# Performance work log

Hardware: AMD Instinct MI355X
Metric: run time of the kernel (lower is better)

Reference implementation:

```python
import jax, jax.numpy as jnp
import numpy as np

TOP_K = 2
LN_EPS = 1e-6


def setup_inputs() -> dict:
    key = jax.random.key(0)
    ks = jax.random.split(key, 8)
    B, T, D, FF, E = 4, 512, 1024, 4096, 8
    x = jax.random.normal(ks[0], (B, T, D), dtype=jnp.float32)
    gate_w = jax.random.normal(ks[1], (E, D), dtype=jnp.float32) * (1.0 / np.sqrt(D))
    ln_g = jnp.ones((E, D), dtype=jnp.float32)
    ln_b = jnp.zeros((E, D), dtype=jnp.float32)
    w1 = jax.random.normal(ks[2], (E, FF, D), dtype=jnp.float32) * (1.0 / np.sqrt(D))
    b1 = jnp.zeros((E, FF), dtype=jnp.float32)
    w2 = jax.random.normal(ks[3], (E, D, FF), dtype=jnp.float32) * (1.0 / np.sqrt(FF))
    b2 = jnp.zeros((E, D), dtype=jnp.float32)
    return {"x": x, "gate_w": gate_w, "ln_g": ln_g, "ln_b": ln_b,
            "w1": w1, "b1": b1, "w2": w2, "b2": b2}


def reference(x, gate_w, ln_g, ln_b, w1, b1, w2, b2):
    B, T, D = x.shape
    E = gate_w.shape[0]
    N = B * T
    xf = x.reshape(N, D)

    # ---- Router: linear gate -> softmax -> top-k dispatch mask + aux loss ----
    logits = xf @ gate_w.T                          # [N, E]
    scores = jax.nn.softmax(logits, axis=-1)        # [N, E]
    topk_vals, topk_idx = jax.lax.top_k(scores, TOP_K)
    dispatch = jnp.zeros_like(scores).at[
        jnp.arange(N)[:, None], topk_idx].set(1.0)  # [N, E] 0/1 mask
    load = dispatch.sum(axis=0)                     # [E]
    importance = scores.sum(axis=0)                 # [E]
    aux_loss = (importance * load).sum() * E / (N * N)

    # ---- Experts (PositionwiseFeedForward, kernel_size=1, skip connection) ----
    # Dense-all-experts compute, masked combine: identical math to the
    # per-expert gather/scatter loop in the torch module.
    mu = xf.mean(axis=-1, keepdims=True)
    var = ((xf - mu) ** 2).mean(axis=-1, keepdims=True)
    norm = (xf - mu) / jnp.sqrt(var + LN_EPS)       # [N, D]
    xe = norm[:, None, :] * ln_g[None] + ln_b[None] # [N, E, D] per-expert LN
    h = jax.nn.relu(jnp.einsum('ned,efd->nef', xe, w1) + b1[None])  # [N, E, FF]
    y = jnp.einsum('nef,edf->ned', h, w2) + b2[None] + xf[:, None, :]  # +skip

    comb = scores * dispatch                        # top-k gate weights [N, E]
    out = jnp.einsum('ne,ned->nd', comb, y).reshape(B, T, D)
    return out, aux_loss
```

## Files before the change

### kernel.cpp

```cpp
#include <hip/hip_runtime.h>
#include <hip/hip_bf16.h>

#define N_TOK 2048
#define DMODEL 1024
#define NEXP 8
#define FFDIM 4096
#define NMAX 2048
#define PADROWS 5120
#define TMAX 40

#define BM 128
#define BN 128
#define BK 64
#define KSPL 4

typedef __attribute__((ext_vector_type(8))) short s16x8;
typedef __attribute__((ext_vector_type(4))) float f32x4;

__device__ __forceinline__ float bf2f(ushort u) {
    union { uint i; float f; } x; x.i = ((uint)u) << 16; return x.f;
}
__device__ __forceinline__ ushort f2bf(float f) {
    union { float f; uint i; } x; x.f = f;
    uint r = x.i + 0x7fffu + ((x.i >> 16) & 1u);
    return (ushort)(r >> 16);
}

__device__ __forceinline__ void gl_lds16(const void* g, void* l) {
    __builtin_amdgcn_global_load_lds(
        (const __attribute__((address_space(1))) unsigned int*)g,
        (__attribute__((address_space(3))) unsigned int*)l, 16, 0, 0);
}

__device__ __forceinline__ float block_sum(float v, float* s4) {
    #pragma unroll
    for (int off = 32; off; off >>= 1) v += __shfl_down(v, off);
    __syncthreads();
    if ((threadIdx.x & 63) == 0) s4[threadIdx.x >> 6] = v;
    __syncthreads();
    return s4[0] + s4[1] + s4[2] + s4[3];
}

__global__ __launch_bounds__(256)
void router_kernel(const float* __restrict__ x, const float* __restrict__ gate_w,
                   ushort* __restrict__ norm, float* __restrict__ scores,
                   int* __restrict__ cnt, int* __restrict__ lists,
                   int4* __restrict__ info, float2* __restrict__ gpair) {
    __shared__ float s4[4];
    const int n = blockIdx.x, tid = threadIdx.x;
    const float* xr = x + (size_t)n * DMODEL;
    float4 v = *(const float4*)(xr + tid * 4);

    float tot = block_sum(v.x + v.y + v.z + v.w, s4);
    float mu = tot * (1.0f / DMODEL);
    float d0 = v.x - mu, d1 = v.y - mu, d2 = v.z - mu, d3 = v.w - mu;
    float var = block_sum(d0 * d0 + d1 * d1 + d2 * d2 + d3 * d3, s4) * (1.0f / DMODEL);
    float rstd = rsqrtf(var + 1e-6f);

    ushort nb[4] = { f2bf(d0 * rstd), f2bf(d1 * rstd), f2bf(d2 * rstd), f2bf(d3 * rstd) };
    *(uint2*)(norm + (size_t)n * DMODEL + tid * 4) = *(uint2*)nb;

    float lg[NEXP];
    #pragma unroll
    for (int e = 0; e < NEXP; ++e) {
        float4 g = *(const float4*)(gate_w + (size_t)e * DMODEL + tid * 4);
        lg[e] = v.x * g.x + v.y * g.y + v.z * g.z + v.w * g.w;
    }
    #pragma unroll
    for (int e = 0; e < NEXP; ++e) lg[e] = block_sum(lg[e], s4);

    if (tid == 0) {
        float m = lg[0];
        #pragma unroll
        for (int e = 1; e < NEXP; ++e) m = fmaxf(m, lg[e]);
        float ex[NEXP], Z = 0.f;
        #pragma unroll
        for (int e = 0; e < NEXP; ++e) { ex[e] = expf(lg[e] - m); Z += ex[e]; }
        float inv = 1.0f / Z;
        float sc[NEXP];
        #pragma unroll
        for (int e = 0; e < NEXP; ++e) { sc[e] = ex[e] * inv; scores[n * NEXP + e] = sc[e]; }
        int i1 = 0;
        #pragma unroll
        for (int e = 1; e < NEXP; ++e) if (sc[e] > sc[i1]) i1 = e;
        int i2 = (i1 == 0) ? 1 : 0;
        #pragma unroll
        for (int e = 0; e < NEXP; ++e) if (e != i1 && sc[e] > sc[i2]) i2 = e;
        int s1 = atomicAdd(&cnt[i1], 1);
        lists[i1 * NMAX + s1] = n;
        int s2 = atomicAdd(&cnt[i2], 1);
        lists[i2 * NMAX + s2] = n;
        info[n] = make_int4(i1, s1, i2, s2);
        gpair[n] = make_float2(sc[i1], sc[i2]);
    }
}

__global__ __launch_bounds__(256)
void prep_kernel(const float* __restrict__ scores, const int* __restrict__ cnt,
                 int* __restrict__ offs_pad, int* __restrict__ ntiles,
                 int4* __restrict__ tilemap, float* __restrict__ aux_out) {
    __shared__ float s4[4];
    __shared__ float imp[NEXP];
    float part[NEXP] = {};
    for (int i = threadIdx.x; i < N_TOK; i += 256) {
        #pragma unroll
        for (int e = 0; e < NEXP; ++e) part[e] += scores[i * NEXP + e];
    }
    #pragma unroll
    for (int e = 0; e < NEXP; ++e) {
        float s = block_sum(part[e], s4);
        if (threadIdx.x == 0) imp[e] = s;
    }
    __syncthreads();
    if (threadIdx.x == 0) {
        float aux = 0.f; int pad = 0, idx = 0;
        #pragma unroll
        for (int e = 0; e < NEXP; ++e) {
            aux += imp[e] * (float)cnt[e];
            offs_pad[e] = pad;
            int tiles = (cnt[e] + BM - 1) / BM;
            for (int t = 0; t < tiles; ++t)
                tilemap[idx++] = make_int4(e, pad + t * BM, 0, 0);
            pad += tiles * BM;
        }
        offs_pad[NEXP] = pad;
        ntiles[0] = idx;
        aux_out[0] = aux * (float)NEXP / ((float)N_TOK * (float)N_TOK);
    }
}

__global__ __launch_bounds__(256)
void gather_kernel(const ushort* __restrict__ norm, const float* __restrict__ ln_g,
                   const float* __restrict__ ln_b, const int* __restrict__ offs_pad,
                   const int* __restrict__ cnt, const int* __restrict__ lists,
                   ushort* __restrict__ A1) {
    const int r = blockIdx.x;
    int e = 0;
    #pragma unroll
    for (int k = 1; k < NEXP; ++k) if (r >= offs_pad[k]) e = k;
    const int slot = r - offs_pad[e];
    const int t4 = threadIdx.x * 4;
    if (slot >= cnt[e]) {
        ushort z[4] = {};
        *(uint2*)(A1 + (size_t)r * DMODEL + t4) = *(uint2*)z;
        return;
    }
    const int token = lists[e * NMAX + slot];
    uint2 nbv = *(const uint2*)(norm + (size_t)token * DMODEL + t4);
    ushort ns[4]; *(uint2*)ns = nbv;
    float4 gv = *(const float4*)(ln_g + (size_t)e * DMODEL + t4);
    float4 bv = *(const float4*)(ln_b + (size_t)e * DMODEL + t4);
    ushort ob[4] = { f2bf(bf2f(ns[0]) * gv.x + bv.x), f2bf(bf2f(ns[1]) * gv.y + bv.y),
                     f2bf(bf2f(ns[2]) * gv.z + bv.z), f2bf(bf2f(ns[3]) * gv.w + bv.w) };
    *(uint2*)(A1 + (size_t)r * DMODEL + t4) = *(uint2*)ob;
}

template<int KDIM, int NT, int KSPLT, bool RELU>
__global__ __launch_bounds__(256, 2)
void moe_gemm(const ushort* __restrict__ A, const float* __restrict__ W,
              const float* __restrict__ bias, const int* __restrict__ ntiles,
              const int4* __restrict__ tilemap, ushort* __restrict__ hout,
              float* __restrict__ yout) {
    __shared__ ushort As[2][BM * BK];
    __shared__ ushort Ws[2][BN * BK];
    constexpr int NOUT = NT * BN;

    const int q = (int)gridDim.x >> 3;
    const int logical = ((int)blockIdx.x & 7) * q + ((int)blockIdx.x >> 3);
    const int bt = logical % TMAX;
    int g = logical / TMAX;
    if (bt >= ntiles[0]) return;
    const int nt = g % NT;
    const int kb = g / NT;
    const int4 tm = tilemap[bt];
    const int e = tm.x, row0 = tm.y;

    const int tid = threadIdx.x, lane = tid & 63, wave = tid >> 6;
    const int wm = (wave & 1) * 64, wn = (wave >> 1) * 64;
    const int trow = lane >> 3;
    const int scol = ((lane & 7) ^ trow) * 8;

    const ushort* Agb = A + (size_t)row0 * KDIM;
    const float*  Wgb = W + ((size_t)e * NOUT + nt * BN) * KDIM;

    f32x4 acc[4][4] = {};
    float4 wr[8];

    auto loadWreg = [&](int step) {
        #pragma unroll
        for (int i = 0; i < 4; ++i) {
            int c = tid + 256 * i;
            const float* p = Wgb + (size_t)(c >> 3) * KDIM + step * BK + (c & 7) * 8;
            wr[2 * i]     = *(const float4*)p;
            wr[2 * i + 1] = *(const float4*)(p + 4);
        }
    };
    auto stageA = [&](int step, int b) {
        #pragma unroll
        for (int i = 0; i < 4; ++i) {
            int c = wave * 4 + i;
            gl_lds16(Agb + (size_t)(c * 8 + trow) * KDIM + step * BK + scol, &As[b][c * 512]);
        }
    };
    auto cvtWriteW = [&](int b) {
        #pragma unroll
        for (int i = 0; i < 4; ++i) {
            int c = tid + 256 * i;
            int row = c >> 3, col8 = (c & 7) * 8;
            union { s16x8 v; __hip_bfloat162 h2[4]; } u;
            u.h2[0] = __float22bfloat162_rn(make_float2(wr[2 * i].x, wr[2 * i].y));
            u.h2[1] = __float22bfloat162_rn(make_float2(wr[2 * i].z, wr[2 * i].w));
            u.h2[2] = __float22bfloat162_rn(make_float2(wr[2 * i + 1].x, wr[2 * i + 1].y));
            u.h2[3] = __float22bfloat162_rn(make_float2(wr[2 * i + 1].z, wr[2 * i + 1].w));
            *(s16x8*)&Ws[b][row * BK + (col8 ^ ((row & 7) << 3))] = u.v;
        }
    };
    auto mfma_phase = [&](int b) {
        #pragma unroll
        for (int kki = 0; kki < 2; ++kki) {
            const int cx = (kki * 32 + (lane >> 4) * 8) ^ ((lane & 7) << 3);
            s16x8 af[4], bfv[4];
            #pragma unroll
            for (int mi = 0; mi < 4; ++mi)
                af[mi] = *(const s16x8*)&As[b][(wm + mi * 16 + (lane & 15)) * BK + cx];
            #pragma unroll
            for (int ni = 0; ni < 4; ++ni)
                bfv[ni] = *(const s16x8*)&Ws[b][(wn + ni * 16 + (lane & 15)) * BK + cx];
            #pragma unroll
            for (int mi = 0; mi < 4; ++mi)
                #pragma unroll
                for (int ni = 0; ni < 4; ++ni)
                    acc[mi][ni] = __builtin_amdgcn_mfma_f32_16x16x32_bf16(
                        af[mi], bfv[ni], acc[mi][ni], 0, 0, 0);
        }
    };

    const int KS = KDIM / BK / KSPLT;
    const int kt0 = kb * KS;

    loadWreg(kt0);
    stageA(kt0, 0);
    cvtWriteW(0);
    asm volatile("s_waitcnt vmcnt(0) lgkmcnt(0)" ::: "memory");
    __builtin_amdgcn_s_barrier();
    __builtin_amdgcn_sched_barrier(0);

    int buf = 0;
    for (int s = 0; s < KS; ++s) {
        if (s + 1 < KS) {
            loadWreg(kt0 + s + 1);
            __builtin_amdgcn_sched_barrier(0);
            stageA(kt0 + s + 1, buf ^ 1);
            __builtin_amdgcn_sched_barrier(0);
        }
        mfma_phase(buf);
        __builtin_amdgcn_sched_barrier(0);
        if (s + 1 < KS) cvtWriteW(buf ^ 1);
        asm volatile("s_waitcnt vmcnt(0) lgkmcnt(0)" ::: "memory");
        __builtin_amdgcn_sched_barrier(0);
        __builtin_amdgcn_s_barrier();
        __builtin_amdgcn_sched_barrier(0);
        buf ^= 1;
    }

    if (RELU) {
        #pragma unroll
        for (int ni = 0; ni < 4; ++ni) {
            const int nn = nt * BN + wn + ni * 16 + (lane & 15);
            const float bv = bias[(size_t)e * NOUT + nn];
            #pragma unroll
            for (int mi = 0; mi < 4; ++mi)
                #pragma unroll
                for (int r = 0; r < 4; ++r) {
                    const int sl = wm + mi * 16 + ((lane >> 4) << 2) + r;
                    hout[(size_t)(row0 + sl) * NOUT + nn] =
                        f2bf(fmaxf(acc[mi][ni][r] + bv, 0.f));
                }
        }
    } else {
        #pragma unroll
        for (int ni = 0; ni < 4; ++ni) {
            const int nn = nt * BN + wn + ni * 16 + (lane & 15);
            #pragma unroll
            for (int mi = 0; mi < 4; ++mi)
                #pragma unroll
                for (int r = 0; r < 4; ++r) {
                    const int sl = wm + mi * 16 + ((lane >> 4) << 2) + r;
                    yout[((size_t)kb * PADROWS + row0 + sl) * NOUT + nn] = acc[mi][ni][r];
                }
        }
    }
}

__global__ __launch_bounds__(256)
void combine_kernel(const float* __restrict__ ypart, const float* __restrict__ b2,
                    const float* __restrict__ x, const int* __restrict__ offs_pad,
                    const int4* __restrict__ info, const float2* __restrict__ gpair,
                    float* __restrict__ out) {
    const int n = blockIdx.x, d = threadIdx.x * 4;
    const int4 ii = info[n];
    const float2 g = gpair[n];
    const int r1 = offs_pad[ii.x] + ii.y, r2 = offs_pad[ii.z] + ii.w;
    f32x4 y1 = {}, y2 = {};
    #pragma unroll
    for (int kb = 0; kb < KSPL; ++kb) {
        y1 += *(const f32x4*)(ypart + ((size_t)kb * PADROWS + r1) * DMODEL + d);
        y2 += *(const f32x4*)(ypart + ((size_t)kb * PADROWS + r2) * DMODEL + d);
    }
    const f32x4 b21 = *(const f32x4*)(b2 + (size_t)ii.x * DMODEL + d);
    const f32x4 b22 = *(const f32x4*)(b2 + (size_t)ii.z * DMODEL + d);
    const f32x4 xv  = *(const f32x4*)(x + (size_t)n * DMODEL + d);
    f32x4 o = g.x * (y1 + b21 + xv) + g.y * (y2 + b22 + xv);
    *(f32x4*)(out + (size_t)n * DMODEL + d) = o;
}

extern "C" void kernel_launch(void* const* d_in, const int* in_sizes, int n_in,
                              void* d_out, int out_size, void* d_ws, size_t ws_size,
                              hipStream_t stream) {
    const float* x      = (const float*)d_in[0];
    const float* gate_w = (const float*)d_in[1];
    const float* ln_g   = (const float*)d_in[2];
    const float* ln_b   = (const float*)d_in[3];
    const float* w1     = (const float*)d_in[4];
    const float* b1     = (const float*)d_in[5];
    const float* w2     = (const float*)d_in[6];
    const float* b2     = (const float*)d_in[7];
    float* out = (float*)d_out;

    char* w = (char*)d_ws;
    int*    cnt      = (int*)(w + 0);
    int*    offs_pad = (int*)(w + 64);
    int*    ntiles   = (int*)(w + 128);
    int4*   tilemap  = (int4*)(w + 192);
    int*    lists    = (int*)(w + 1024);
    float*  scores   = (float*)(w + 66560);
    int4*   info     = (int4*)(w + 132096);
    float2* gpair    = (float2*)(w + 164864);
    ushort* norm     = (ushort*)(w + 181248);
    ushort* A1       = (ushort*)(w + 4375552);
    ushort* h        = (ushort*)(w + 14861312);
    float*  ypart    = (float*)(w + 56804352);

    hipMemsetAsync(cnt, 0, 64, stream);

    router_kernel<<<N_TOK, 256, 0, stream>>>(x, gate_w, norm, scores, cnt, lists, info, gpair);
    prep_kernel<<<1, 256, 0, stream>>>(scores, cnt, offs_pad, ntiles, tilemap,
                                       out + (size_t)N_TOK * DMODEL);
    gather_kernel<<<PADROWS, 256, 0, stream>>>(norm, ln_g, ln_b, offs_pad, cnt, lists, A1);
    moe_gemm<DMODEL, FFDIM / BN, 1, true><<<TMAX * (FFDIM / BN), 256, 0, stream>>>(
        A1, w1, b1, ntiles, tilemap, h, nullptr);
    moe_gemm<FFDIM, DMODEL / BN, KSPL, false><<<TMAX * (DMODEL / BN) * KSPL, 256, 0, stream>>>(
        h, w2, nullptr, ntiles, tilemap, nullptr, ypart);
    combine_kernel<<<N_TOK, 256, 0, stream>>>(ypart, b2, x, offs_pad, info, gpair, out);
}
```

Measured before the change: 299.6 us.

## Stream fp32 weights straight to LDS and convert at fragment read; one token per wave in router

The GEMM no longer loads fp32 weights into registers and converts them before writing to LDS. It stages them directly into swizzled fp32 LDS with global_load_lds and converts to bf16 when building MFMA fragments. BK is halved to 32 so the fp32 tile fits, occupancy is raised to 3 blocks per CU, and the prefetch now waits with a partial vmcnt so it overlaps the MFMA phase. The router handles one token per wave with shuffle reductions in place of block-level barriers. The trade-off is more k-steps, more barriers per unit of work, and a conversion inside the MFMA loop.

```diff
diff --git a/kernel.cpp b/kernel.cpp
--- a/kernel.cpp
+++ b/kernel.cpp
@@ -11,7 +11,7 @@
 
 #define BM 128
 #define BN 128
-#define BK 64
+#define BK 32
 #define KSPL 4
 
 typedef __attribute__((ext_vector_type(8))) short s16x8;
@@ -30,6 +30,12 @@
     __builtin_amdgcn_global_load_lds(
         (const __attribute__((address_space(1))) unsigned int*)g,
         (__attribute__((address_space(3))) unsigned int*)l, 16, 0, 0);
+}
+
+__device__ __forceinline__ float wave_sum(float v) {
+    #pragma unroll
+    for (int off = 32; off; off >>= 1) v += __shfl_xor(v, off);
+    return v;
 }
 
 __device__ __forceinline__ float block_sum(float v, float* s4) {
@@ -46,30 +52,52 @@
                    ushort* __restrict__ norm, float* __restrict__ scores,
                    int* __restrict__ cnt, int* __restrict__ lists,
                    int4* __restrict__ info, float2* __restrict__ gpair) {
-    __shared__ float s4[4];
-    const int n = blockIdx.x, tid = threadIdx.x;
-    const float* xr = x + (size_t)n * DMODEL;
-    float4 v = *(const float4*)(xr + tid * 4);
-
-    float tot = block_sum(v.x + v.y + v.z + v.w, s4);
-    float mu = tot * (1.0f / DMODEL);
-    float d0 = v.x - mu, d1 = v.y - mu, d2 = v.z - mu, d3 = v.w - mu;
-    float var = block_sum(d0 * d0 + d1 * d1 + d2 * d2 + d3 * d3, s4) * (1.0f / DMODEL);
-    float rstd = rsqrtf(var + 1e-6f);
-
-    ushort nb[4] = { f2bf(d0 * rstd), f2bf(d1 * rstd), f2bf(d2 * rstd), f2bf(d3 * rstd) };
-    *(uint2*)(norm + (size_t)n * DMODEL + tid * 4) = *(uint2*)nb;
+    const int wave = threadIdx.x >> 6, lane = threadIdx.x & 63;
+    const int n = blockIdx.x * 4 + wave;
+    const float* xr = x + (size_t)n * DMODEL + lane * 16;
+
+    float4 v[4];
+    #pragma unroll
+    for (int j = 0; j < 4; ++j) v[j] = *(const float4*)(xr + j * 4);
+
+    float s = 0.f;
+    #pragma unroll
+    for (int j = 0; j < 4; ++j) s += v[j].x + v[j].y + v[j].z + v[j].w;
+    const float mu = wave_sum(s) * (1.0f / DMODEL);
+
+    float vs = 0.f;
+    #pragma unroll
+    for (int j = 0; j < 4; ++j) {
+        float a = v[j].x - mu, b = v[j].y - mu, c = v[j].z - mu, d = v[j].w - mu;
+        vs += a * a + b * b + c * c + d * d;
+    }
+    const float rstd = rsqrtf(wave_sum(vs) * (1.0f / DMODEL) + 1e-6f);
+
+    ushort nb[16];
+    #pragma unroll
+    for (int j = 0; j < 4; ++j) {
+        nb[j * 4 + 0] = f2bf((v[j].x - mu) * rstd);
+        nb[j * 4 + 1] = f2bf((v[j].y - mu) * rstd);
+        nb[j * 4 + 2] = f2bf((v[j].z - mu) * rstd);
+        nb[j * 4 + 3] = f2bf((v[j].w - mu) * rstd);
+    }
+    *(uint4*)(norm + (size_t)n * DMODEL + lane * 16)     = *(uint4*)&nb[0];
+    *(uint4*)(norm + (size_t)n * DMODEL + lane * 16 + 8) = *(uint4*)&nb[8];
 
     float lg[NEXP];
     #pragma unroll
     for (int e = 0; e < NEXP; ++e) {
-        float4 g = *(const float4*)(gate_w + (size_t)e * DMODEL + tid * 4);
-        lg[e] = v.x * g.x + v.y * g.y + v.z * g.z + v.w * g.w;
-    }
-    #pragma unroll
-    for (int e = 0; e < NEXP; ++e) lg[e] = block_sum(lg[e], s4);
-
-    if (tid == 0) {
+        const float* gw = gate_w + (size_t)e * DMODEL + lane * 16;
+        float acc = 0.f;
+        #pragma unroll
+        for (int j = 0; j < 4; ++j) {
+            float4 g = *(const float4*)(gw + j * 4);
+            acc += v[j].x * g.x + v[j].y * g.y + v[j].z * g.z + v[j].w * g.w;
+        }
+        lg[e] = wave_sum(acc);
+    }
+
+    if (lane == 0) {
         float m = lg[0];
         #pragma unroll
         for (int e = 1; e < NEXP; ++e) m = fmaxf(m, lg[e]);
@@ -156,13 +184,13 @@
 }
 
 template<int KDIM, int NT, int KSPLT, bool RELU>
-__global__ __launch_bounds__(256, 2)
+__global__ __launch_bounds__(256, 3)
 void moe_gemm(const ushort* __restrict__ A, const float* __restrict__ W,
               const float* __restrict__ bias, const int* __restrict__ ntiles,
               const int4* __restrict__ tilemap, ushort* __restrict__ hout,
               float* __restrict__ yout) {
     __shared__ ushort As[2][BM * BK];
-    __shared__ ushort Ws[2][BN * BK];
+    __shared__ float  Wsf[2][BN * BK];
     constexpr int NOUT = NT * BN;
 
     const int q = (int)gridDim.x >> 3;
@@ -177,91 +205,87 @@
 
     const int tid = threadIdx.x, lane = tid & 63, wave = tid >> 6;
     const int wm = (wave & 1) * 64, wn = (wave >> 1) * 64;
-    const int trow = lane >> 3;
-    const int scol = ((lane & 7) ^ trow) * 8;
 
     const ushort* Agb = A + (size_t)row0 * KDIM;
     const float*  Wgb = W + ((size_t)e * NOUT + nt * BN) * KDIM;
 
     f32x4 acc[4][4] = {};
-    float4 wr[8];
-
-    auto loadWreg = [&](int step) {
+
+    auto stageA = [&](int step, int b) {
+        #pragma unroll
+        for (int i = 0; i < 2; ++i) {
+            const int c = wave * 128 + i * 64 + lane;
+            const int row = c >> 2;
+            const int src = ((c & 3) ^ (row & 3)) * 8;
+            gl_lds16(Agb + (size_t)row * KDIM + step * BK + src,
+                     &As[b][(wave * 128 + i * 64) * 8]);
+        }
+    };
+    auto stageW = [&](int step, int b) {
         #pragma unroll
         for (int i = 0; i < 4; ++i) {
-            int c = tid + 256 * i;
-            const float* p = Wgb + (size_t)(c >> 3) * KDIM + step * BK + (c & 7) * 8;
-            wr[2 * i]     = *(const float4*)p;
-            wr[2 * i + 1] = *(const float4*)(p + 4);
+            const int c = wave * 256 + i * 64 + lane;
+            const int row = c >> 3;
+            const int src = ((c & 7) ^ (row & 7)) * 4;
+            gl_lds16(Wgb + (size_t)row * KDIM + step * BK + src,
+                     &Wsf[b][(wave * 256 + i * 64) * 4]);
         }
     };
-    auto stageA = [&](int step, int b) {
-        #pragma unroll
-        for (int i = 0; i < 4; ++i) {
-            int c = wave * 4 + i;
-            gl_lds16(Agb + (size_t)(c * 8 + trow) * KDIM + step * BK + scol, &As[b][c * 512]);
-        }
-    };
-    auto cvtWriteW = [&](int b) {
-        #pragma unroll
-        for (int i = 0; i < 4; ++i) {
-            int c = tid + 256 * i;
-            int row = c >> 3, col8 = (c & 7) * 8;
-            union { s16x8 v; __hip_bfloat162 h2[4]; } u;
-            u.h2[0] = __float22bfloat162_rn(make_float2(wr[2 * i].x, wr[2 * i].y));
-            u.h2[1] = __float22bfloat162_rn(make_float2(wr[2 * i].z, wr[2 * i].w));
-            u.h2[2] = __float22bfloat162_rn(make_float2(wr[2 * i + 1].x, wr[2 * i + 1].y));
-            u.h2[3] = __float22bfloat162_rn(make_float2(wr[2 * i + 1].z, wr[2 * i + 1].w));
-            *(s16x8*)&Ws[b][row * BK + (col8 ^ ((row & 7) << 3))] = u.v;
-        }
+    auto readW = [&](int b, int ni) -> s16x8 {
+        const int row = wn + ni * 16 + (lane & 15);
+        const int x = row & 7;
+        const int cb = (lane >> 4) * 2;
+        const float4 f0 = *(const float4*)&Wsf[b][row * BK + ((cb ^ x) << 2)];
+        const float4 f1 = *(const float4*)&Wsf[b][row * BK + (((cb + 1) ^ x) << 2)];
+        union { s16x8 v; __hip_bfloat162 h2[4]; } u;
+        u.h2[0] = __float22bfloat162_rn(make_float2(f0.x, f0.y));
+        u.h2[1] = __float22bfloat162_rn(make_float2(f0.z, f0.w));
+        u.h2[2] = __float22bfloat162_rn(make_float2(f1.x, f1.y));
+        u.h2[3] = __float22bfloat162_rn(make_float2(f1.z, f1.w));
+        return u.v;
     };
     auto mfma_phase = [&](int b) {
-        #pragma unroll
-        for (int kki = 0; kki < 2; ++kki) {
-            const int cx = (kki * 32 + (lane >> 4) * 8) ^ ((lane & 7) << 3);
-            s16x8 af[4], bfv[4];
-            #pragma unroll
-            for (int mi = 0; mi < 4; ++mi)
-                af[mi] = *(const s16x8*)&As[b][(wm + mi * 16 + (lane & 15)) * BK + cx];
+        s16x8 af[4], bfv[4];
+        #pragma unroll
+        for (int mi = 0; mi < 4; ++mi) {
+            const int row = wm + mi * 16 + (lane & 15);
+            af[mi] = *(const s16x8*)&As[b][row * BK + (((lane >> 4) ^ (row & 3)) * 8)];
+        }
+        #pragma unroll
+        for (int ni = 0; ni < 4; ++ni)
+            bfv[ni] = readW(b, ni);
+        #pragma unroll
+        for (int mi = 0; mi < 4; ++mi)
             #pragma unroll
             for (int ni = 0; ni < 4; ++ni)
-                bfv[ni] = *(const s16x8*)&Ws[b][(wn + ni * 16 + (lane & 15)) * BK + cx];
-            #pragma unroll
-            for (int mi = 0; mi < 4; ++mi)
-                #pragma unroll
-                for (int ni = 0; ni < 4; ++ni)
-                    acc[mi][ni] = __builtin_amdgcn_mfma_f32_16x16x32_bf16(
-                        af[mi], bfv[ni], acc[mi][ni], 0, 0, 0);
-        }
+                acc[mi][ni] = __builtin_amdgcn_mfma_f32_16x16x32_bf16(
+                    af[mi], bfv[ni], acc[mi][ni], 0, 0, 0);
     };
 
     const int KS = KDIM / BK / KSPLT;
     const int kt0 = kb * KS;
 
-    loadWreg(kt0);
     stageA(kt0, 0);
-    cvtWriteW(0);
-    asm volatile("s_waitcnt vmcnt(0) lgkmcnt(0)" ::: "memory");
-    __builtin_amdgcn_s_barrier();
+    stageW(kt0, 0);
     __builtin_amdgcn_sched_barrier(0);
 
     int buf = 0;
     for (int s = 0; s < KS; ++s) {
-        if (s + 1 < KS) {
-            loadWreg(kt0 + s + 1);
-            __builtin_amdgcn_sched_barrier(0);
-            stageA(kt0 + s + 1, buf ^ 1);
-            __builtin_amdgcn_sched_barrier(0);
-        }
+        const int nxt = (s + 1 < KS) ? (kt0 + s + 1) : (kt0 + s);
+        stageA(nxt, buf ^ 1);
+        stageW(nxt, buf ^ 1);
+        __builtin_amdgcn_sched_barrier(0);
+        asm volatile("s_waitcnt vmcnt(6)" ::: "memory");
+        __builtin_amdgcn_sched_barrier(0);
+        __builtin_amdgcn_s_barrier();
+        __builtin_amdgcn_sched_barrier(0);
         mfma_phase(buf);
         __builtin_amdgcn_sched_barrier(0);
-        if (s + 1 < KS) cvtWriteW(buf ^ 1);
-        asm volatile("s_waitcnt vmcnt(0) lgkmcnt(0)" ::: "memory");
-        __builtin_amdgcn_sched_barrier(0);
         __builtin_amdgcn_s_barrier();
         __builtin_amdgcn_sched_barrier(0);
         buf ^= 1;
     }
+    asm volatile("s_waitcnt vmcnt(0)" ::: "memory");
 
     if (RELU) {
         #pragma unroll
@@ -343,7 +367,7 @@
 
     hipMemsetAsync(cnt, 0, 64, stream);
 
-    router_kernel<<<N_TOK, 256, 0, stream>>>(x, gate_w, norm, scores, cnt, lists, info, gpair);
+    router_kernel<<<N_TOK / 4, 256, 0, stream>>>(x, gate_w, norm, scores, cnt, lists, info, gpair);
     prep_kernel<<<1, 256, 0, stream>>>(scores, cnt, offs_pad, ntiles, tilemap,
                                        out + (size_t)N_TOK * DMODEL);
     gather_kernel<<<PADROWS, 256, 0, stream>>>(norm, ln_g, ln_b, offs_pad, cnt, lists, A1);
```

New measurement: 283.8 us. -5.3%, faster.
